# Kernel tuning notes

Measured on AMD Instinct MI355X. Metric: run time of the kernel, lower is better.

Reference implementation:

```python
import jax, jax.numpy as jnp
import numpy as np

C = 512
C8 = C // 8   # query/key dim = 64
C2 = C // 2   # value dim = 256


def setup_inputs() -> dict:
    key = jax.random.key(0)
    ks = jax.random.split(key, 10)
    B, H, W = 4, 64, 64
    x = jax.random.normal(ks[0], (B, H, W, C), dtype=jnp.float32)
    # 1x1 conv kernels expressed as [in_ch, out_ch] matrices + biases
    Wf = jax.random.normal(ks[1], (C, C8), dtype=jnp.float32) * 0.02
    bf = jnp.zeros((C8,), dtype=jnp.float32)
    Wg = jax.random.normal(ks[2], (C, C8), dtype=jnp.float32) * 0.02
    bg = jnp.zeros((C8,), dtype=jnp.float32)
    Wh = jax.random.normal(ks[3], (C, C2), dtype=jnp.float32) * 0.02
    bh = jnp.zeros((C2,), dtype=jnp.float32)
    Wo = jax.random.normal(ks[4], (C2, C), dtype=jnp.float32) * 0.02
    bo = jnp.zeros((C,), dtype=jnp.float32)
    gamma = jax.random.normal(ks[5], (1,), dtype=jnp.float32) * 0.05
    return {"x": x, "Wf": Wf, "bf": bf, "Wg": Wg, "bg": bg,
            "Wh": Wh, "bh": bh, "Wo": Wo, "bo": bo, "gamma": gamma}


def reference(x, Wf, bf, Wg, bg, Wh, bh, Wo, bo, gamma):
    B, H, W, _ = x.shape
    N = H * W
    xf = x.reshape(B, N, C)                               # flatten spatial dims
    f = xf @ Wf + bf                                      # [B, N, C8] keys
    g = xf @ Wg + bg                                      # [B, N, C8] queries
    h = xf @ Wh + bh                                      # [B, N, C2] values
    s = jnp.einsum('bnd,bmd->bnm', g, f)                  # [B, N, N] scores (g @ f^T)
    beta = jax.nn.softmax(s, axis=-1)                     # attention map
    o = jnp.einsum('bnm,bmd->bnd', beta, h)               # [B, N, C2]
    o = o @ Wo + bo                                       # [B, N, C] output 1x1 conv
    out = gamma * o + xf                                  # residual with learned scale
    return out.reshape(B, H, W, C)
```

## Files before the change

kernel.cpp:

```cpp
#include <hip/hip_runtime.h>
#include <math.h>

#define B_   4
#define N_   4096
#define C_   512
#define C8_  64
#define C2_  256

typedef __attribute__((ext_vector_type(8))) short bf16x8;
typedef __attribute__((ext_vector_type(4))) short bf16x4;
typedef __attribute__((ext_vector_type(4))) float floatx4;
typedef __attribute__((ext_vector_type(16))) float floatx16;

__device__ __forceinline__ short f2bf(float x) {
    unsigned u = __float_as_uint(x);
    u += 0x7fff + ((u >> 16) & 1);
    return (short)(u >> 16);
}
__device__ __forceinline__ unsigned pack2bf(float a, float b) {
    return (unsigned)(unsigned short)f2bf(a) | ((unsigned)(unsigned short)f2bf(b) << 16);
}

union U8 { bf16x8 v; unsigned u[4]; };

__global__ __launch_bounds__(256) void convert_w(
    const float* __restrict__ Wf, const float* __restrict__ Wg,
    const float* __restrict__ Wh, const float* __restrict__ Wo,
    short* __restrict__ WcatT, short* __restrict__ WoT)
{
    int tid = blockIdx.x * 256 + threadIdx.x;
    if (tid < 384 * 512) {
        int n = tid >> 9, k = tid & 511;
        float v = (n < 64)  ? Wf[k * 64 + n]
                : (n < 128) ? Wg[k * 64 + (n - 64)]
                            : Wh[k * 256 + (n - 128)];
        WcatT[tid] = f2bf(v);
    } else {
        int t2 = tid - 384 * 512;
        int n = t2 >> 8, k = t2 & 255;
        WoT[t2] = f2bf(Wo[k * 512 + n]);
    }
}

__global__ __launch_bounds__(256, 2) void qkv_mfma(
    const float* __restrict__ x, const short* __restrict__ WcatT,
    const float* __restrict__ bfv, const float* __restrict__ bgv,
    const float* __restrict__ bhv,
    short* __restrict__ fbf, short* __restrict__ gbf, short* __restrict__ hT)
{
    const int ny = blockIdx.x;
    const int m0 = blockIdx.y * 128;
    const int n0 = ny * 128;
    const int t  = threadIdx.x;
    const int w  = t >> 6, lane = t & 63;
    const int l15 = lane & 15, quad = lane >> 4;
    const int wm = w & 1, wn = w >> 1;

    __shared__ short As[128 * 40];
    __shared__ short Bs[128 * 40];

    floatx4 acc[4][4];
    #pragma unroll
    for (int i = 0; i < 4; i++)
        #pragma unroll
        for (int j = 0; j < 4; j++) acc[i][j] = (floatx4){0.f,0.f,0.f,0.f};

    for (int k0 = 0; k0 < C_; k0 += 32) {
        #pragma unroll
        for (int i = 0; i < 4; i++) {
            int c = t + i * 256;
            int row = c >> 3, ko = (c & 7) * 4;
            float4 v = *(const float4*)&x[(size_t)(m0 + row) * C_ + k0 + ko];
            bf16x4 pk = { f2bf(v.x), f2bf(v.y), f2bf(v.z), f2bf(v.w) };
            *(bf16x4*)&As[row * 40 + ko] = pk;
        }
        #pragma unroll
        for (int i = 0; i < 2; i++) {
            int c = t + i * 256;
            int nr = c >> 2, ko = (c & 3) * 8;
            *(bf16x8*)&Bs[nr * 40 + ko] =
                *(const bf16x8*)&WcatT[(size_t)(n0 + nr) * 512 + k0 + ko];
        }
        __syncthreads();

        bf16x8 af[4], bfr[4];
        #pragma unroll
        for (int mt = 0; mt < 4; mt++)
            af[mt] = *(const bf16x8*)&As[(wm * 64 + mt * 16 + l15) * 40 + quad * 8];
        #pragma unroll
        for (int nt = 0; nt < 4; nt++)
            bfr[nt] = *(const bf16x8*)&Bs[(wn * 64 + nt * 16 + l15) * 40 + quad * 8];
        #pragma unroll
        for (int mt = 0; mt < 4; mt++)
            #pragma unroll
            for (int nt = 0; nt < 4; nt++)
                acc[mt][nt] = __builtin_amdgcn_mfma_f32_16x16x32_bf16(af[mt], bfr[nt], acc[mt][nt], 0, 0, 0);
        __syncthreads();
    }

    if (ny == 0) {
        #pragma unroll
        for (int mt = 0; mt < 4; mt++) {
            #pragma unroll
            for (int nt = 0; nt < 4; nt++) {
                int cn = wn * 64 + nt * 16 + l15;
                #pragma unroll
                for (int rg = 0; rg < 4; rg++) {
                    int row = m0 + wm * 64 + mt * 16 + quad * 4 + rg;
                    float v = acc[mt][nt][rg];
                    if (cn < 64) fbf[(size_t)row * 64 + cn]        = f2bf(v + bfv[cn]);
                    else         gbf[(size_t)row * 64 + (cn - 64)] = f2bf(v + bgv[cn - 64]);
                }
            }
        }
    } else {
        #pragma unroll
        for (int mt = 0; mt < 4; mt++) {
            #pragma unroll
            for (int nt = 0; nt < 4; nt++) {
                int hch = (ny - 1) * 128 + wn * 64 + nt * 16 + l15;
                int row = m0 + wm * 64 + mt * 16 + quad * 4;
                int bb = row >> 12, n = row & 4095;
                float bias = bhv[hch];
                bf16x4 pk = { f2bf(acc[mt][nt][0] + bias), f2bf(acc[mt][nt][1] + bias),
                              f2bf(acc[mt][nt][2] + bias), f2bf(acc[mt][nt][3] + bias) };
                *(bf16x4*)&hT[((size_t)(bb * 256 + hch)) * 4096 + n] = pk;
            }
        }
    }
}

#define HST 40

__global__ __launch_bounds__(256, 1) void attn_v3(
    const short* __restrict__ fK,
    const short* __restrict__ gQ,
    const short* __restrict__ hT,
    float* __restrict__ oPart,
    float* __restrict__ lPart)
{
    const int bx = blockIdx.x;
    const int s  = bx & 1;
    const int qt = (bx >> 1) & 31;
    const int b  = bx >> 6;
    const int kb = s * 2048;
    const int t  = threadIdx.x;
    const int w  = t >> 6, lane = t & 63;
    const int l31 = lane & 31, h = lane >> 5;
    const int wq = w & 1, wv = w >> 1;
    const int q_wave = qt * 128 + wq * 64;

    __shared__ short fs[2][64 * HST];
    __shared__ short hs[2][256 * HST];

    bf16x8 qf[2][4];
    #pragma unroll
    for (int n2 = 0; n2 < 2; n2++)
        #pragma unroll
        for (int k = 0; k < 4; k++)
            qf[n2][k] = *(const bf16x8*)&gQ[(size_t)(b * N_ + q_wave + n2 * 32 + l31) * 64 + k * 16 + h * 8];

    floatx16 oacc[2][4];
    #pragma unroll
    for (int n2 = 0; n2 < 2; n2++)
        #pragma unroll
        for (int vt = 0; vt < 4; vt++)
            #pragma unroll
            for (int j = 0; j < 16; j++) oacc[n2][vt][j] = 0.f;
    float lsum[2] = {0.f, 0.f};

    const int f_row = t >> 2, f_c = (t & 3) * 16;
    const int h_row = t >> 3, h_c = (t & 7) * 8;

    {
        *(bf16x8*)&fs[0][f_row * HST + f_c] =
            *(const bf16x8*)&fK[(size_t)(b * N_ + kb + f_row) * 64 + f_c];
        *(bf16x8*)&fs[0][f_row * HST + f_c + 8] =
            *(const bf16x8*)&fK[(size_t)(b * N_ + kb + f_row) * 64 + f_c + 8];
        #pragma unroll
        for (int i = 0; i < 8; i++)
            *(bf16x8*)&hs[0][(h_row + i * 32) * HST + h_c] =
                *(const bf16x8*)&hT[((size_t)(b * 256 + h_row + i * 32)) * 4096 + kb + h_c];
    }
    __syncthreads();

    for (int it = 0; it < 32; ++it) {
        const int cur = it & 1;
        const bool more = (it < 31);
        const int kn = kb + (it + 1) * 64;

        bf16x8 rf0, rf1, rh[8];
        if (more) {
            rf0 = *(const bf16x8*)&fK[(size_t)(b * N_ + kn + f_row) * 64 + f_c];
            rf1 = *(const bf16x8*)&fK[(size_t)(b * N_ + kn + f_row) * 64 + f_c + 8];
            #pragma unroll
            for (int i = 0; i < 8; i++)
                rh[i] = *(const bf16x8*)&hT[((size_t)(b * 256 + h_row + i * 32)) * 4096 + kn + h_c];
        }

        bf16x8 ffr[2][4];
        #pragma unroll
        for (int m = 0; m < 2; m++)
            #pragma unroll
            for (int k = 0; k < 4; k++)
                ffr[m][k] = *(const bf16x8*)&fs[cur][(m * 32 + l31) * HST + k * 16 + h * 8];

        floatx16 sacc[2][2];
        #pragma unroll
        for (int m = 0; m < 2; m++)
            #pragma unroll
            for (int n2 = 0; n2 < 2; n2++) {
                #pragma unroll
                for (int j = 0; j < 16; j++) sacc[m][n2][j] = 0.f;
                #pragma unroll
                for (int k = 0; k < 4; k++)
                    sacc[m][n2] = __builtin_amdgcn_mfma_f32_32x32x16_bf16(
                        ffr[m][k], qf[n2][k], sacc[m][n2], 0, 0, 0);
            }

        bf16x8 pfrag[2][4];
        #pragma unroll
        for (int m = 0; m < 2; m++)
            #pragma unroll
            for (int n2 = 0; n2 < 2; n2++) {
                float p[16]; float ps_ = 0.f;
                #pragma unroll
                for (int j = 0; j < 16; j++) { p[j] = __expf(sacc[m][n2][j]); ps_ += p[j]; }
                ps_ += __shfl_xor(ps_, 32);
                lsum[n2] += ps_;
                unsigned pk[8], xk[8];
                #pragma unroll
                for (int i = 0; i < 8; i++) pk[i] = pack2bf(p[2 * i], p[2 * i + 1]);
                #pragma unroll
                for (int i = 0; i < 8; i++) xk[i] = __shfl_xor(pk[i], 32);
                #pragma unroll
                for (int kp = 0; kp < 2; kp++) {
                    U8 u;
                    u.u[0] = h ? xk[4 * kp + 2] : pk[4 * kp];
                    u.u[1] = h ? xk[4 * kp + 3] : pk[4 * kp + 1];
                    u.u[2] = h ? pk[4 * kp + 2] : xk[4 * kp];
                    u.u[3] = h ? pk[4 * kp + 3] : xk[4 * kp + 1];
                    pfrag[n2][m * 2 + kp] = u.v;
                }
            }

        #pragma unroll
        for (int kk = 0; kk < 4; kk++)
            #pragma unroll
            for (int vt = 0; vt < 4; vt++) {
                bf16x8 vfr = *(const bf16x8*)&hs[cur][(wv * 128 + vt * 32 + l31) * HST + kk * 16 + h * 8];
                #pragma unroll
                for (int n2 = 0; n2 < 2; n2++)
                    oacc[n2][vt] = __builtin_amdgcn_mfma_f32_32x32x16_bf16(
                        pfrag[n2][kk], vfr, oacc[n2][vt], 0, 0, 0);
            }

        if (more) {
            const int nxt = cur ^ 1;
            *(bf16x8*)&fs[nxt][f_row * HST + f_c] = rf0;
            *(bf16x8*)&fs[nxt][f_row * HST + f_c + 8] = rf1;
            #pragma unroll
            for (int i = 0; i < 8; i++)
                *(bf16x8*)&hs[nxt][(h_row + i * 32) * HST + h_c] = rh[i];
        }
        __syncthreads();
    }

    #pragma unroll
    for (int n2 = 0; n2 < 2; n2++) {
        #pragma unroll
        for (int vt = 0; vt < 4; vt++) {
            int vch = wv * 128 + vt * 32 + l31;
            #pragma unroll
            for (int r = 0; r < 16; r++) {
                int q = q_wave + n2 * 32 + (r & 3) + 8 * (r >> 2) + 4 * h;
                oPart[(size_t)s * 4194304 + (size_t)(b * N_ + q) * 256 + vch] = oacc[n2][vt][r];
            }
        }
    }
    if (wv == 0 && lane < 32) {
        #pragma unroll
        for (int n2 = 0; n2 < 2; n2++)
            lPart[(size_t)s * 16384 + b * N_ + q_wave + n2 * 32 + lane] = lsum[n2];
    }
}

__global__ __launch_bounds__(256) void attn_combine(
    const float* __restrict__ oPart, const float* __restrict__ lPart,
    short* __restrict__ obf)
{
    int idx = blockIdx.x * 256 + threadIdx.x;
    int row = idx >> 6;
    int c4  = (idx & 63) << 2;
    float4 a = *(const float4*)&oPart[(size_t)row * 256 + c4];
    float4 b = *(const float4*)&oPart[4194304 + (size_t)row * 256 + c4];
    float inv = 1.0f / (lPart[row] + lPart[16384 + row]);
    bf16x4 o = { f2bf((a.x + b.x) * inv), f2bf((a.y + b.y) * inv),
                 f2bf((a.z + b.z) * inv), f2bf((a.w + b.w) * inv) };
    *(bf16x4*)&obf[(size_t)row * 256 + c4] = o;
}

__global__ __launch_bounds__(256, 2) void out_mfma(
    const short* __restrict__ obf, const short* __restrict__ WoT,
    const float* __restrict__ bo, const float* __restrict__ x,
    const float* __restrict__ gamma, float* __restrict__ out)
{
    const int n0 = blockIdx.x * 128;
    const int m0 = blockIdx.y * 128;
    const int t  = threadIdx.x;
    const int w  = t >> 6, lane = t & 63;
    const int l15 = lane & 15, quad = lane >> 4;
    const int wm = w & 1, wn = w >> 1;

    __shared__ short As[128 * 40];
    __shared__ short Bs[128 * 40];

    floatx4 acc[4][4];
    #pragma unroll
    for (int i = 0; i < 4; i++)
        #pragma unroll
        for (int j = 0; j < 4; j++) acc[i][j] = (floatx4){0.f,0.f,0.f,0.f};

    for (int k0 = 0; k0 < C2_; k0 += 32) {
        #pragma unroll
        for (int i = 0; i < 2; i++) {
            int c = t + i * 256;
            int row = c >> 2, ko = (c & 3) * 8;
            *(bf16x8*)&As[row * 40 + ko] =
                *(const bf16x8*)&obf[(size_t)(m0 + row) * 256 + k0 + ko];
        }
        #pragma unroll
        for (int i = 0; i < 2; i++) {
            int c = t + i * 256;
            int nr = c >> 2, ko = (c & 3) * 8;
            *(bf16x8*)&Bs[nr * 40 + ko] =
                *(const bf16x8*)&WoT[(size_t)(n0 + nr) * 256 + k0 + ko];
        }
        __syncthreads();

        bf16x8 af[4], bfr[4];
        #pragma unroll
        for (int mt = 0; mt < 4; mt++)
            af[mt] = *(const bf16x8*)&As[(wm * 64 + mt * 16 + l15) * 40 + quad * 8];
        #pragma unroll
        for (int nt = 0; nt < 4; nt++)
            bfr[nt] = *(const bf16x8*)&Bs[(wn * 64 + nt * 16 + l15) * 40 + quad * 8];
        #pragma unroll
        for (int mt = 0; mt < 4; mt++)
            #pragma unroll
            for (int nt = 0; nt < 4; nt++)
                acc[mt][nt] = __builtin_amdgcn_mfma_f32_16x16x32_bf16(af[mt], bfr[nt], acc[mt][nt], 0, 0, 0);
        __syncthreads();
    }

    const float gm = gamma[0];
    #pragma unroll
    for (int mt = 0; mt < 4; mt++) {
        #pragma unroll
        for (int nt = 0; nt < 4; nt++) {
            int col = n0 + wn * 64 + nt * 16 + l15;
            float bias = bo[col];
            #pragma unroll
            for (int rg = 0; rg < 4; rg++) {
                int row = m0 + wm * 64 + mt * 16 + quad * 4 + rg;
                out[(size_t)row * C_ + col] =
                    gm * (acc[mt][nt][rg] + bias) + x[(size_t)row * C_ + col];
            }
        }
    }
}

extern "C" void kernel_launch(void* const* d_in, const int* in_sizes, int n_in,
                              void* d_out, int out_size, void* d_ws, size_t ws_size,
                              hipStream_t stream) {
    (void)in_sizes; (void)n_in; (void)out_size; (void)ws_size;

    const float* x     = (const float*)d_in[0];
    const float* Wf    = (const float*)d_in[1];
    const float* bfv   = (const float*)d_in[2];
    const float* Wg    = (const float*)d_in[3];
    const float* bgv   = (const float*)d_in[4];
    const float* Wh    = (const float*)d_in[5];
    const float* bhv   = (const float*)d_in[6];
    const float* Wo    = (const float*)d_in[7];
    const float* bo    = (const float*)d_in[8];
    const float* gamma = (const float*)d_in[9];
    float* out = (float*)d_out;

    short* fbf   = (short*)d_ws;
    short* gbf   = fbf   + (size_t)B_ * N_ * C8_;
    short* hT    = gbf   + (size_t)B_ * N_ * C8_;
    short* obf   = hT    + (size_t)B_ * C2_ * N_;
    short* WcatT = obf   + (size_t)B_ * N_ * C2_;
    short* WoT   = WcatT + (size_t)384 * 512;
    float* oPart = (float*)(WoT + (size_t)512 * 256);
    float* lPart = oPart + (size_t)2 * 16384 * 256;

    convert_w<<<1280, 256, 0, stream>>>(Wf, Wg, Wh, Wo, WcatT, WoT);
    qkv_mfma<<<dim3(3, 128), 256, 0, stream>>>(x, WcatT, bfv, bgv, bhv, fbf, gbf, hT);
    attn_v3<<<256, 256, 0, stream>>>(fbf, gbf, hT, oPart, lPart);
    attn_combine<<<4096, 256, 0, stream>>>(oPart, lPart, obf);
    out_mfma<<<dim3(4, 128), 256, 0, stream>>>(obf, WoT, bo, x, gamma, out);
}
```

Baseline: 232.7 us.

## Split attention keys four ways, use exp2, hardware bf16 packing, and permlane swaps

When the workspace is large enough, the attention kernel splits the key range into four chunks instead of two, which doubles the grid, and allows two blocks per CU through launch bounds. The combine kernel now reduces a variable number of partials. The query projection is pre-scaled by log2(e) so the softmax can use a native exp2. Bf16 packing switches to v_cvt_pk_bf16_f32, and the half-wave exchange of the P fragments uses permlane32_swap instead of shuffles. The MFMA sections are wrapped in s_setprio. The cost is more partial-output traffic and register pressure from the second block per CU.

```diff
diff --git a/kernel.cpp b/kernel.cpp
--- a/kernel.cpp
+++ b/kernel.cpp
@@ -6,22 +6,27 @@
 #define C_   512
 #define C8_  64
 #define C2_  256
+#define LOG2E 1.4426950408889634f
 
 typedef __attribute__((ext_vector_type(8))) short bf16x8;
 typedef __attribute__((ext_vector_type(4))) short bf16x4;
 typedef __attribute__((ext_vector_type(4))) float floatx4;
 typedef __attribute__((ext_vector_type(16))) float floatx16;
+typedef __attribute__((ext_vector_type(2))) unsigned uint32x2;
 
 __device__ __forceinline__ short f2bf(float x) {
     unsigned u = __float_as_uint(x);
     u += 0x7fff + ((u >> 16) & 1);
     return (short)(u >> 16);
 }
-__device__ __forceinline__ unsigned pack2bf(float a, float b) {
-    return (unsigned)(unsigned short)f2bf(a) | ((unsigned)(unsigned short)f2bf(b) << 16);
+__device__ __forceinline__ unsigned cvtpk(float a, float b) {
+    unsigned r;
+    asm("v_cvt_pk_bf16_f32 %0, %1, %2" : "=v"(r) : "v"(a), "v"(b));
+    return r;
 }
 
 union U8 { bf16x8 v; unsigned u[4]; };
+union U4 { bf16x4 v; unsigned u[2]; };
 
 __global__ __launch_bounds__(256) void convert_w(
     const float* __restrict__ Wf, const float* __restrict__ Wg,
@@ -71,8 +76,8 @@
             int c = t + i * 256;
             int row = c >> 3, ko = (c & 7) * 4;
             float4 v = *(const float4*)&x[(size_t)(m0 + row) * C_ + k0 + ko];
-            bf16x4 pk = { f2bf(v.x), f2bf(v.y), f2bf(v.z), f2bf(v.w) };
-            *(bf16x4*)&As[row * 40 + ko] = pk;
+            U4 pk; pk.u[0] = cvtpk(v.x, v.y); pk.u[1] = cvtpk(v.z, v.w);
+            *(bf16x4*)&As[row * 40 + ko] = pk.v;
         }
         #pragma unroll
         for (int i = 0; i < 2; i++) {
@@ -109,7 +114,7 @@
                     int row = m0 + wm * 64 + mt * 16 + quad * 4 + rg;
                     float v = acc[mt][nt][rg];
                     if (cn < 64) fbf[(size_t)row * 64 + cn]        = f2bf(v + bfv[cn]);
-                    else         gbf[(size_t)row * 64 + (cn - 64)] = f2bf(v + bgv[cn - 64]);
+                    else         gbf[(size_t)row * 64 + (cn - 64)] = f2bf((v + bgv[cn - 64]) * LOG2E);
                 }
             }
         }
@@ -122,9 +127,10 @@
                 int row = m0 + wm * 64 + mt * 16 + quad * 4;
                 int bb = row >> 12, n = row & 4095;
                 float bias = bhv[hch];
-                bf16x4 pk = { f2bf(acc[mt][nt][0] + bias), f2bf(acc[mt][nt][1] + bias),
-                              f2bf(acc[mt][nt][2] + bias), f2bf(acc[mt][nt][3] + bias) };
-                *(bf16x4*)&hT[((size_t)(bb * 256 + hch)) * 4096 + n] = pk;
+                U4 pk;
+                pk.u[0] = cvtpk(acc[mt][nt][0] + bias, acc[mt][nt][1] + bias);
+                pk.u[1] = cvtpk(acc[mt][nt][2] + bias, acc[mt][nt][3] + bias);
+                *(bf16x4*)&hT[((size_t)(bb * 256 + hch)) * 4096 + n] = pk.v;
             }
         }
     }
@@ -132,18 +138,20 @@
 
 #define HST 40
 
-__global__ __launch_bounds__(256, 1) void attn_v3(
+__global__ __launch_bounds__(256, 2) void attn_v4(
     const short* __restrict__ fK,
     const short* __restrict__ gQ,
     const short* __restrict__ hT,
     float* __restrict__ oPart,
-    float* __restrict__ lPart)
+    float* __restrict__ lPart,
+    int sbits)
 {
     const int bx = blockIdx.x;
-    const int s  = bx & 1;
-    const int qt = (bx >> 1) & 31;
-    const int b  = bx >> 6;
-    const int kb = s * 2048;
+    const int s  = bx & ((1 << sbits) - 1);
+    const int qt = (bx >> sbits) & 31;
+    const int b  = bx >> (sbits + 5);
+    const int kb = s << (12 - sbits);
+    const int niter = 64 >> sbits;
     const int t  = threadIdx.x;
     const int w  = t >> 6, lane = t & 63;
     const int l31 = lane & 31, h = lane >> 5;
@@ -184,9 +192,9 @@
     }
     __syncthreads();
 
-    for (int it = 0; it < 32; ++it) {
+    for (int it = 0; it < niter; ++it) {
         const int cur = it & 1;
-        const bool more = (it < 31);
+        const bool more = (it < niter - 1);
         const int kn = kb + (it + 1) * 64;
 
         bf16x8 rf0, rf1, rh[8];
@@ -206,6 +214,7 @@
                 ffr[m][k] = *(const bf16x8*)&fs[cur][(m * 32 + l31) * HST + k * 16 + h * 8];
 
         floatx16 sacc[2][2];
+        __builtin_amdgcn_s_setprio(1);
         #pragma unroll
         for (int m = 0; m < 2; m++)
             #pragma unroll
@@ -217,6 +226,7 @@
                     sacc[m][n2] = __builtin_amdgcn_mfma_f32_32x32x16_bf16(
                         ffr[m][k], qf[n2][k], sacc[m][n2], 0, 0, 0);
             }
+        __builtin_amdgcn_s_setprio(0);
 
         bf16x8 pfrag[2][4];
         #pragma unroll
@@ -225,25 +235,25 @@
             for (int n2 = 0; n2 < 2; n2++) {
                 float p[16]; float ps_ = 0.f;
                 #pragma unroll
-                for (int j = 0; j < 16; j++) { p[j] = __expf(sacc[m][n2][j]); ps_ += p[j]; }
+                for (int j = 0; j < 16; j++) {
+                    p[j] = __builtin_amdgcn_exp2f(sacc[m][n2][j]);
+                    ps_ += p[j];
+                }
                 ps_ += __shfl_xor(ps_, 32);
                 lsum[n2] += ps_;
-                unsigned pk[8], xk[8];
-                #pragma unroll
-                for (int i = 0; i < 8; i++) pk[i] = pack2bf(p[2 * i], p[2 * i + 1]);
-                #pragma unroll
-                for (int i = 0; i < 8; i++) xk[i] = __shfl_xor(pk[i], 32);
+                unsigned pk[8];
+                #pragma unroll
+                for (int i = 0; i < 8; i++) pk[i] = cvtpk(p[2 * i], p[2 * i + 1]);
                 #pragma unroll
                 for (int kp = 0; kp < 2; kp++) {
-                    U8 u;
-                    u.u[0] = h ? xk[4 * kp + 2] : pk[4 * kp];
-                    u.u[1] = h ? xk[4 * kp + 3] : pk[4 * kp + 1];
-                    u.u[2] = h ? pk[4 * kp + 2] : xk[4 * kp];
-                    u.u[3] = h ? pk[4 * kp + 3] : xk[4 * kp + 1];
+                    uint32x2 r0 = __builtin_amdgcn_permlane32_swap(pk[4 * kp],     pk[4 * kp + 2], false, false);
+                    uint32x2 r1 = __builtin_amdgcn_permlane32_swap(pk[4 * kp + 1], pk[4 * kp + 3], false, false);
+                    U8 u; u.u[0] = r0[0]; u.u[1] = r1[0]; u.u[2] = r0[1]; u.u[3] = r1[1];
                     pfrag[n2][m * 2 + kp] = u.v;
                 }
             }
 
+        __builtin_amdgcn_s_setprio(1);
         #pragma unroll
         for (int kk = 0; kk < 4; kk++)
             #pragma unroll
@@ -254,6 +264,7 @@
                     oacc[n2][vt] = __builtin_amdgcn_mfma_f32_32x32x16_bf16(
                         pfrag[n2][kk], vfr, oacc[n2][vt], 0, 0, 0);
             }
+        __builtin_amdgcn_s_setprio(0);
 
         if (more) {
             const int nxt = cur ^ 1;
@@ -287,17 +298,23 @@
 
 __global__ __launch_bounds__(256) void attn_combine(
     const float* __restrict__ oPart, const float* __restrict__ lPart,
-    short* __restrict__ obf)
+    short* __restrict__ obf, int nsplit)
 {
     int idx = blockIdx.x * 256 + threadIdx.x;
     int row = idx >> 6;
     int c4  = (idx & 63) << 2;
     float4 a = *(const float4*)&oPart[(size_t)row * 256 + c4];
-    float4 b = *(const float4*)&oPart[4194304 + (size_t)row * 256 + c4];
-    float inv = 1.0f / (lPart[row] + lPart[16384 + row]);
-    bf16x4 o = { f2bf((a.x + b.x) * inv), f2bf((a.y + b.y) * inv),
-                 f2bf((a.z + b.z) * inv), f2bf((a.w + b.w) * inv) };
-    *(bf16x4*)&obf[(size_t)row * 256 + c4] = o;
+    float l = lPart[row];
+    for (int s2 = 1; s2 < nsplit; s2++) {
+        float4 bv = *(const float4*)&oPart[(size_t)s2 * 4194304 + (size_t)row * 256 + c4];
+        a.x += bv.x; a.y += bv.y; a.z += bv.z; a.w += bv.w;
+        l += lPart[(size_t)s2 * 16384 + row];
+    }
+    float inv = 1.0f / l;
+    U4 o;
+    o.u[0] = cvtpk(a.x * inv, a.y * inv);
+    o.u[1] = cvtpk(a.z * inv, a.w * inv);
+    *(bf16x4*)&obf[(size_t)row * 256 + c4] = o.v;
 }
 
 __global__ __launch_bounds__(256, 2) void out_mfma(
@@ -373,7 +390,7 @@
 extern "C" void kernel_launch(void* const* d_in, const int* in_sizes, int n_in,
                               void* d_out, int out_size, void* d_ws, size_t ws_size,
                               hipStream_t stream) {
-    (void)in_sizes; (void)n_in; (void)out_size; (void)ws_size;
+    (void)in_sizes; (void)n_in; (void)out_size;
 
     const float* x     = (const float*)d_in[0];
     const float* Wf    = (const float*)d_in[1];
@@ -394,11 +411,17 @@
     short* WcatT = obf   + (size_t)B_ * N_ * C2_;
     short* WoT   = WcatT + (size_t)384 * 512;
     float* oPart = (float*)(WoT + (size_t)512 * 256);
-    float* lPart = oPart + (size_t)2 * 16384 * 256;
+
+    const size_t base_bytes = ((size_t)2 * 1048576 + 4194304 + 4194304 + 196608 + 131072) * 2;
+    const size_t need4 = base_bytes + 4ull * (16777216 + 65536);
+    const int sbits  = (ws_size >= need4) ? 2 : 1;
+    const int nsplit = 1 << sbits;
+
+    float* lPart = oPart + (size_t)nsplit * 16384 * 256;
 
     convert_w<<<1280, 256, 0, stream>>>(Wf, Wg, Wh, Wo, WcatT, WoT);
     qkv_mfma<<<dim3(3, 128), 256, 0, stream>>>(x, WcatT, bfv, bgv, bhv, fbf, gbf, hT);
-    attn_v3<<<256, 256, 0, stream>>>(fbf, gbf, hT, oPart, lPart);
-    attn_combine<<<4096, 256, 0, stream>>>(oPart, lPart, obf);
+    attn_v4<<<128 << sbits, 256, 0, stream>>>(fbf, gbf, hT, oPart, lPart, sbits);
+    attn_combine<<<4096, 256, 0, stream>>>(oPart, lPart, obf, nsplit);
     out_mfma<<<dim3(4, 128), 256, 0, stream>>>(obf, WoT, bo, x, gamma, out);
 }
```

Result: slower. 337.4 us (+45.0%).
